# Performance work log

Measured on AMD Instinct MI355X. Metric: run time of the kernel, lower is better.

## Reference

```python
import jax, jax.numpy as jnp
import numpy as np

B, D, L, T, K = 16, 256, 256, 1000, 3
DW, DC = 4, 2  # dim_w, dim_c
CH = 8         # ConvSwishBlock out channels (10 = 1 start + 1 end + 8)


def swish(x):
    return x * jax.nn.sigmoid(x)


def setup_inputs() -> dict:
    key = jax.random.key(0)
    ks = jax.random.split(key, 12)
    # durations ~ U[1,6] per phone -> sum ~ 3.5*L ~ 896 <= T
    durations = 1.0 + 5.0 * jax.random.uniform(ks[0], (B, L), dtype=jnp.float32)
    phoneme = jax.random.normal(ks[1], (B, D, L), dtype=jnp.float32)
    # True = padded phone position
    phone_len = L - (jnp.arange(B) % 4) * 16
    phoneme_mask = (jnp.arange(L)[None, :] >= phone_len[:, None])[:, None, :]
    durations = jnp.where(phoneme_mask[:, 0, :], 0.0, durations)
    s = 0.02
    p = {
        'proj_w_W': s * jax.random.normal(ks[2], (D, D)), 'proj_w_b': jnp.zeros((D,)),
        'conv_w_W': s * jax.random.normal(ks[3], (CH, D, K)), 'conv_w_b': jnp.zeros((CH,)),
        'mlp_w_W': s * jax.random.normal(ks[4], (2 + CH, DW)), 'mlp_w_b': jnp.zeros((DW,)),
        'lin_w_W': s * jax.random.normal(ks[5], (D * DW, D)), 'lin_w_b': jnp.zeros((D,)),
        'proj_c_W': s * jax.random.normal(ks[6], (D, D)), 'proj_c_b': jnp.zeros((D,)),
        'conv_c_W': s * jax.random.normal(ks[7], (CH, D, K)), 'conv_c_b': jnp.zeros((CH,)),
        'mlp_c_W': s * jax.random.normal(ks[8], (2 + CH, DC)), 'mlp_c_b': jnp.zeros((DC,)),
        'lin_c_W': s * jax.random.normal(ks[9], (DW * DC, D)), 'lin_c_b': jnp.zeros((D,)),
    }
    return {'durations': durations, 'phoneme': phoneme, 'phoneme_mask': phoneme_mask, **p}


def _conv_branch(x, phone_pad, projW, projb, convW, convb):
    # x: (B, D, L). 1x1 conv projection, then K-wide 'same' conv to CH channels, swish, mask.
    x = jnp.einsum('od,bdl->bol', projW, x) + projb[None, :, None]
    h = jax.lax.conv_general_dilated(x, convW, (1,), 'SAME',
                                     dimension_numbers=('NCH', 'OIH', 'NCH'))
    h = swish(h + convb[None, :, None])
    h = jnp.where(phone_pad[:, None, :], 0.0, h)
    return h.transpose(0, 2, 1)  # (B, L, CH)


def _forward(durations, phoneme, phoneme_mask,
             proj_w_W, proj_w_b, conv_w_W, conv_w_b, mlp_w_W, mlp_w_b, lin_w_W, lin_w_b,
             proj_c_W, proj_c_b, conv_c_W, conv_c_b, mlp_c_W, mlp_c_b, lin_c_W, lin_c_b):
    phone_pad = phoneme_mask[:, 0, :]                       # (B, L) True = pad
    frame_len = jnp.clip(jnp.round(jnp.sum(durations, -1)), 0, T).astype(jnp.int32)
    frame_pad = jnp.arange(T)[None, :] >= frame_len[:, None]  # (B, T) True = pad
    attn_pad = frame_pad[:, :, None] | phone_pad[:, None, :]  # (B, T, L)

    sd = jnp.cumsum(durations, -1)                          # (B, L) cumulative end times
    sk = sd - durations                                     # (B, L) start times
    t = jnp.arange(1, T + 1, dtype=durations.dtype)
    S = jnp.where(attn_pad, 0.0, t[None, :, None] - sk[:, None, :])                    # (B,T,L)
    E = jnp.where(attn_pad, 0.0, jnp.broadcast_to(sd[:, None, :], attn_pad.shape)
                  - sk[:, None, :])                                                    # (B,T,L)

    # W branch: per-(frame, phone) attention weights over phones
    h_w = _conv_branch(phoneme, phone_pad, proj_w_W, proj_w_b, conv_w_W, conv_w_b)     # (B,L,CH)
    feat_w = jnp.concatenate(
        [S[..., None], E[..., None], jnp.broadcast_to(h_w[:, None], (B, T, L, CH))], -1)
    w = swish(feat_w @ mlp_w_W + mlp_w_b)                   # (B, T, L, DW)
    w = jnp.where(phone_pad[:, None, :, None], -jnp.inf, w)
    w = jax.nn.softmax(w, axis=2)                           # softmax over phones
    w = jnp.where(frame_pad[:, :, None, None], 0.0, w)

    # C branch: auxiliary per-(frame, phone) context
    h_c = _conv_branch(phoneme, phone_pad, proj_c_W, proj_c_b, conv_c_W, conv_c_b)
    feat_c = jnp.concatenate(
        [S[..., None], E[..., None], jnp.broadcast_to(h_c[:, None], (B, T, L, CH))], -1)
    c = swish(feat_c @ mlp_c_W + mlp_c_b)                   # (B, T, L, DC)

    # combine: wh = einsum over phones with phoneme features, wc with c matrix
    wh = jnp.einsum('btnq,bnh->btqh', w, phoneme.transpose(0, 2, 1))  # (B,T,DW,D)
    wh = wh.reshape(B, T, DW * D) @ lin_w_W + lin_w_b                 # (B,T,D)
    wc = jnp.einsum('btnq,btnp->btqp', w, c)                          # (B,T,DW,DC)
    wc = wc.reshape(B, T, DW * DC) @ lin_c_W + lin_c_b                # (B,T,D)
    return wh + wc


def reference(durations, phoneme, phoneme_mask,
              proj_w_W, proj_w_b, conv_w_W, conv_w_b, mlp_w_W, mlp_w_b, lin_w_W, lin_w_b,
              proj_c_W, proj_c_b, conv_c_W, conv_c_b, mlp_c_W, mlp_c_b, lin_c_W, lin_c_b):
    return _forward(durations, phoneme, phoneme_mask,
                    proj_w_W, proj_w_b, conv_w_W, conv_w_b, mlp_w_W, mlp_w_b, lin_w_W, lin_w_b,
                    proj_c_W, proj_c_b, conv_c_W, conv_c_b, mlp_c_W, mlp_c_b, lin_c_W, lin_c_b)
```

## Files before the change

### kernel.cpp

```cpp
#include <hip/hip_runtime.h>


typedef short v8s __attribute__((ext_vector_type(8)));
typedef _Float16 v8h __attribute__((ext_vector_type(8)));
typedef float f4 __attribute__((ext_vector_type(4)));

__device__ __forceinline__ float bf2f(unsigned short h) {
  return __uint_as_float(((unsigned int)h) << 16);
}
__device__ __forceinline__ unsigned short f2bf(float f) {
  unsigned int u = __float_as_uint(f);
  u = (u + 0x7FFFu + ((u >> 16) & 1u)) >> 16;
  return (unsigned short)u;
}
__device__ __forceinline__ float swishf(float x) {
  return x * __builtin_amdgcn_rcpf(1.f + __expf(-x));
}

__global__ __launch_bounds__(256) void k_prep(
    const float* __restrict__ dur, const float* __restrict__ ph,
    const float* __restrict__ liWw,
    const float* __restrict__ cvWw, const float* __restrict__ pjWw,
    const float* __restrict__ pjbw,
    const float* __restrict__ cvWc, const float* __restrict__ pjWc,
    const float* __restrict__ pjbc,
    float* __restrict__ sk, int* __restrict__ frame_len,
    unsigned short* __restrict__ Mb, float* __restrict__ bK,
    unsigned short* __restrict__ LWT, unsigned short* __restrict__ phT) {
  __shared__ float sm[32 * 33];
  int blk = blockIdx.x, tid = threadIdx.x;
  if (blk < 16) {
    int b = blk, l = tid;
    float d = dur[b * 256 + l];
    sm[l] = d;
    __syncthreads();
    for (int off = 1; off < 256; off <<= 1) {
      float v = (l >= off) ? sm[l - off] : 0.f;
      __syncthreads();
      sm[l] += v;
      __syncthreads();
    }
    sk[b * 256 + l] = sm[l] - d;
    if (l == 255) {
      int fl = (int)rintf(sm[255]);
      frame_len[b] = min(max(fl, 0), 1000);
    }
  } else if (blk < 64) {
    int x = blk - 16;
    int br = x / 24, ck = x % 24;
    int ch = ck / 3, k = ck % 3;
    const float* convW = br ? cvWc : cvWw;
    const float* projW = br ? pjWc : pjWw;
    const float* projb = br ? pjbc : pjbw;
    int d = tid;
    float acc = 0.f;
    for (int o = 0; o < 256; o++)
      acc += convW[ch * 768 + o * 3 + k] * projW[o * 256 + d];
    Mb[(br * 24 + ck) * 256 + d] = f2bf(acc);
    if (d == 0) {
      float bb = 0.f;
      for (int o = 0; o < 256; o++)
        bb += convW[ch * 768 + o * 3 + k] * projb[o];
      bK[br * 24 + ck] = bb;
    }
  } else if (blk < 320) {
    int idx = blk - 64;
    int kt = idx & 31, ot = idx >> 5;
    int tx = tid & 31, ty = tid >> 5;
#pragma unroll
    for (int r = 0; r < 4; r++) {
      int row = ty + r * 8;
      sm[row * 33 + tx] = liWw[(size_t)(kt * 32 + row) * 256 + ot * 32 + tx];
    }
    __syncthreads();
#pragma unroll
    for (int r = 0; r < 4; r++) {
      int row = ty + r * 8;
      LWT[(size_t)(ot * 32 + row) * 1024 + kt * 32 + tx] =
          f2bf(sm[tx * 33 + row]);
    }
  } else {
    int idx = blk - 320;
    int ht = idx & 7, lt = (idx >> 3) & 7, b = idx >> 6;
    int tx = tid & 31, ty = tid >> 5;
#pragma unroll
    for (int r = 0; r < 4; r++) {
      int row = ty + r * 8;
      sm[row * 33 + tx] =
          ph[(size_t)b * 65536 + (size_t)(ht * 32 + row) * 256 + lt * 32 + tx];
    }
    __syncthreads();
#pragma unroll
    for (int r = 0; r < 4; r++) {
      int row = ty + r * 8;
      phT[(size_t)b * 65536 + (size_t)(lt * 32 + row) * 256 + ht * 32 + tx] =
          f2bf(sm[tx * 33 + row]);
    }
  }
}

__global__ __launch_bounds__(256) void k_convG(
    const unsigned short* __restrict__ phT, const unsigned short* __restrict__ Mb,
    const float* __restrict__ bK, const float* __restrict__ cvbw,
    const float* __restrict__ cvbc, const float* __restrict__ dur,
    const unsigned short* __restrict__ LWT,
    float* __restrict__ hw, float* __restrict__ hc,
    _Float16* __restrict__ G) {
  __shared__ __align__(16) float C[256 * 49];
  int blk = blockIdx.x;
  int tid = threadIdx.x, wave = tid >> 6, lane = tid & 63;
  int quad = lane >> 4, col = lane & 15;
  if (blk < 16) {
    int b = blk;
    int l0 = wave * 64;
    const unsigned short* Ab = phT + (size_t)b * 65536;
    f4 acc[4][3] = {};
#pragma unroll
    for (int k0 = 0; k0 < 256; k0 += 32) {
      v8s af[4], bf[3];
#pragma unroll
      for (int lt = 0; lt < 4; lt++)
        af[lt] = *(const v8s*)(Ab + (size_t)(l0 + lt * 16 + col) * 256 + k0 + quad * 8);
#pragma unroll
      for (int ct = 0; ct < 3; ct++)
        bf[ct] = *(const v8s*)(Mb + (size_t)(ct * 16 + col) * 256 + k0 + quad * 8);
#pragma unroll
      for (int lt = 0; lt < 4; lt++)
#pragma unroll
        for (int ct = 0; ct < 3; ct++)
          acc[lt][ct] = __builtin_amdgcn_mfma_f32_16x16x32_bf16(af[lt], bf[ct],
                                                                acc[lt][ct], 0, 0, 0);
    }
#pragma unroll
    for (int lt = 0; lt < 4; lt++)
#pragma unroll
      for (int ct = 0; ct < 3; ct++)
#pragma unroll
        for (int r = 0; r < 4; r++)
          C[(l0 + lt * 16 + quad * 4 + r) * 49 + ct * 16 + col] = acc[lt][ct][r];
    __syncthreads();
    int l = tid;
    float dv = dur[b * 256 + l];
    bool vld = (dv != 0.f);
#pragma unroll
    for (int br = 0; br < 2; br++) {
      const float* convb = br ? cvbc : cvbw;
      float* dst = br ? hc : hw;
#pragma unroll
      for (int ch = 0; ch < 8; ch++) {
        int ck = br * 24 + ch * 3;
        float v = convb[ch] + bK[ck + 1] + C[l * 49 + ck + 1];
        if (l > 0) v += bK[ck + 0] + C[(l - 1) * 49 + ck + 0];
        if (l < 255) v += bK[ck + 2] + C[(l + 1) * 49 + ck + 2];
        v = swishf(v);
        dst[((size_t)(b * 256 + l)) * 8 + ch] = vld ? v : 0.f;
      }
    }
  } else {
    int idx = blk - 16;
    int b = idx >> 4;
    int sub = idx & 15;
    int q = sub >> 2, quadr = sub & 3;
    int mo = (quadr >> 1) * 128, nl = (quadr & 1) * 128;
    int wm = (wave & 1) * 64, wn = (wave >> 1) * 64;
    const unsigned short* Ag = LWT + (size_t)q * 256;
    const unsigned short* Bg = phT + (size_t)b * 65536;
    f4 acc[4][4] = {};
#pragma unroll
    for (int k0 = 0; k0 < 256; k0 += 32) {
      v8s af[4], bf[4];
#pragma unroll
      for (int mt = 0; mt < 4; mt++)
        af[mt] = *(const v8s*)(Ag + (size_t)(mo + wm + mt * 16 + col) * 1024 +
                               k0 + quad * 8);
#pragma unroll
      for (int nt = 0; nt < 4; nt++)
        bf[nt] = *(const v8s*)(Bg + (size_t)(nl + wn + nt * 16 + col) * 256 +
                               k0 + quad * 8);
#pragma unroll
      for (int mt = 0; mt < 4; mt++)
#pragma unroll
        for (int nt = 0; nt < 4; nt++)
          acc[mt][nt] = __builtin_amdgcn_mfma_f32_16x16x32_bf16(af[mt], bf[nt],
                                                                acc[mt][nt], 0, 0, 0);
    }
    _Float16* Gb = G + (size_t)b * 262144 + q * 256;
#pragma unroll
    for (int mt = 0; mt < 4; mt++)
#pragma unroll
      for (int r = 0; r < 4; r++) {
        int orow = mo + wm + mt * 16 + quad * 4 + r;
#pragma unroll
        for (int nt = 0; nt < 4; nt++) {
          int lcol = nl + wn + nt * 16 + col;
          Gb[(size_t)orow * 1024 + lcol] = (_Float16)acc[mt][nt][r];
        }
      }
  }
}

__global__ __launch_bounds__(256) void k_soft(
    const float* __restrict__ dur, const float* __restrict__ sk,
    const int* __restrict__ frame_len,
    const float* __restrict__ hw, const float* __restrict__ hc,
    const float* __restrict__ mlpWw, const float* __restrict__ mlpbw,
    const float* __restrict__ mlpWc, const float* __restrict__ mlpbc,
    _Float16* __restrict__ w, float* __restrict__ wc) {
  __shared__ __align__(16) float4 Lbw4[272];
  __shared__ __align__(16) float4 Laux4[272];
  __shared__ float4 wredM[4];
  int b = blockIdx.y;
  int t0 = blockIdx.x * 16;
  int tid = threadIdx.x, wave = tid >> 6, lane = tid & 63;

  {
    int l = tid;
    float4 a0 = *(const float4*)&hw[((size_t)(b * 256 + l)) * 8];
    float4 a1 = *(const float4*)&hw[((size_t)(b * 256 + l)) * 8 + 4];
    float4 c0 = *(const float4*)&hc[((size_t)(b * 256 + l)) * 8];
    float4 c1 = *(const float4*)&hc[((size_t)(b * 256 + l)) * 8 + 4];
    float hwv[8] = {a0.x, a0.y, a0.z, a0.w, a1.x, a1.y, a1.z, a1.w};
    float hcv[8] = {c0.x, c0.y, c0.z, c0.w, c1.x, c1.y, c1.z, c1.w};
    float dl = dur[b * 256 + l];
    float skl = sk[b * 256 + l];
    float msk = (dl != 0.f) ? 1.f : 0.f;
    float A[4];
#pragma unroll
    for (int q = 0; q < 4; q++) {
      float a = mlpbw[q] + dl * mlpWw[4 + q] - skl * mlpWw[q];
#pragma unroll
      for (int ch = 0; ch < 8; ch++) a += hwv[ch] * mlpWw[(2 + ch) * 4 + q];
      A[q] = (msk != 0.f) ? a : -1e30f;
    }
    float bb0 = mlpbc[0] + dl * mlpWc[2] - skl * mlpWc[0];
    float bb1 = mlpbc[1] + dl * mlpWc[3] - skl * mlpWc[1];
#pragma unroll
    for (int ch = 0; ch < 8; ch++) {
      bb0 += hcv[ch] * mlpWc[(2 + ch) * 2 + 0];
      bb1 += hcv[ch] * mlpWc[(2 + ch) * 2 + 1];
    }
    int li = l + (l >> 4);
    float4 Av = {A[0], A[1], A[2], A[3]};
    Lbw4[li] = Av;
    float4 xv = {bb0, bb1, msk, 0.f};
    Laux4[li] = xv;
    float m0 = A[0], m1 = A[1], m2 = A[2], m3 = A[3];
#pragma unroll
    for (int off = 1; off < 64; off <<= 1) {
      m0 = fmaxf(m0, __shfl_xor(m0, off));
      m1 = fmaxf(m1, __shfl_xor(m1, off));
      m2 = fmaxf(m2, __shfl_xor(m2, off));
      m3 = fmaxf(m3, __shfl_xor(m3, off));
    }
    if (lane == 0) {
      float4 mv = {m0, m1, m2, m3};
      wredM[wave] = mv;
    }
  }
  __syncthreads();
  float4 W0 = wredM[0], W1 = wredM[1], W2 = wredM[2], W3 = wredM[3];
  float maxA[4] = {fmaxf(fmaxf(W0.x, W1.x), fmaxf(W2.x, W3.x)),
                   fmaxf(fmaxf(W0.y, W1.y), fmaxf(W2.y, W3.y)),
                   fmaxf(fmaxf(W0.z, W1.z), fmaxf(W2.z, W3.z)),
                   fmaxf(fmaxf(W0.w, W1.w), fmaxf(W2.w, W3.w))};

  int fl = frame_len[b];
  int tl = wave * 4 + (lane >> 4);
  int l16 = lane & 15;
  int t = t0 + tl;
  bool live = (t < fl);
  float tp1 = (float)(t + 1);
  float mw0[4] = {mlpWw[0], mlpWw[1], mlpWw[2], mlpWw[3]};
  float mc0 = mlpWc[0], mc1 = mlpWc[1];
  float m[4];
#pragma unroll
  for (int q = 0; q < 4; q++)
    m[q] = live ? fmaxf(maxA[q] + tp1 * mw0[q], 0.f) : 1e30f;

  float s[4] = {}, pw[4][2] = {{}, {}, {}, {}};
  v8h eh[4][2];
  int lbase = l16 * 17;
#pragma unroll
  for (int j = 0; j < 16; j++) {
    float4 A4 = Lbw4[lbase + j];
    float4 ax = Laux4[lbase + j];
    float cp0 = swishf(ax.x + tp1 * mc0);
    float cp1 = swishf(ax.y + tp1 * mc1);
    float Aq[4] = {A4.x, A4.y, A4.z, A4.w};
#pragma unroll
    for (int q = 0; q < 4; q++) {
      float z = Aq[q] + tp1 * mw0[q];
      float e = __expf(swishf(z) - m[q]) * ax.z;
      eh[q][j >> 3][j & 7] = (_Float16)e;
      s[q] += e;
      pw[q][0] += e * cp0;
      pw[q][1] += e * cp1;
    }
  }
#pragma unroll
  for (int off = 1; off < 16; off <<= 1) {
#pragma unroll
    for (int q = 0; q < 4; q++) {
      s[q] += __shfl_xor(s[q], off);
      pw[q][0] += __shfl_xor(pw[q][0], off);
      pw[q][1] += __shfl_xor(pw[q][1], off);
    }
  }
  size_t base = ((size_t)b * 1024 + t) * 1024;
#pragma unroll
  for (int q = 0; q < 4; q++) {
    float iv = live ? __builtin_amdgcn_rcpf(s[q]) : 0.f;
    _Float16 ivh = (_Float16)iv;
    v8h w0 = eh[q][0] * ivh;
    v8h w1 = eh[q][1] * ivh;
    *(v8h*)(w + base + q * 256 + l16 * 16) = w0;
    *(v8h*)(w + base + q * 256 + l16 * 16 + 8) = w1;
    if (l16 == 0 && t < 1000) {
      wc[((size_t)(b * 1000 + t)) * 8 + q * 2 + 0] = pw[q][0] * iv;
      wc[((size_t)(b * 1000 + t)) * 8 + q * 2 + 1] = pw[q][1] * iv;
    }
  }
}

__global__ __launch_bounds__(256) void k_out(const _Float16* __restrict__ w,
                                             const _Float16* __restrict__ G,
                                             const float* __restrict__ lwb,
                                             const float* __restrict__ lcb,
                                             const float* __restrict__ LC,
                                             const float* __restrict__ wc,
                                             float* __restrict__ out) {
  int b = blockIdx.y;
  int t0 = (blockIdx.x >> 1) * 32;
  int o0 = (blockIdx.x & 1) * 128;
  int tid = threadIdx.x, wave = tid >> 6, lane = tid & 63;
  int quad = lane >> 4, col = lane & 15;
  __shared__ __align__(16) _Float16 Asm[32 * 40];
  __shared__ __align__(16) _Float16 Bsm[128 * 40];
  __shared__ float bias_s[128];
  __shared__ float lcs[8][128];
  __shared__ float wcs[32][8];

  for (int i = tid; i < 128; i += 256) bias_s[i] = lwb[o0 + i] + lcb[o0 + i];
  for (int i = tid; i < 1024; i += 256)
    lcs[i >> 7][i & 127] = LC[(i >> 7) * 256 + o0 + (i & 127)];
  {
    int r = tid >> 3, j = tid & 7;
    int t = t0 + r;
    wcs[r][j] = (t < 1000) ? wc[((size_t)(b * 1000 + t)) * 8 + j] : 0.f;
  }

  bool aload = tid < 128;
  int arow = tid >> 2, aseg = tid & 3;
  const _Float16* Ag =
      w + (size_t)b * 1048576 + (size_t)(t0 + arow) * 1024 + aseg * 8;
  _Float16* Al = Asm + arow * 40 + aseg * 8;
  int brow = wave * 32 + (lane >> 2), bseg = lane & 3;
  const _Float16* Bg0 =
      G + (size_t)b * 262144 + (size_t)(o0 + brow) * 1024 + bseg * 8;
  const _Float16* Bg1 = Bg0 + 16 * 1024;
  _Float16* Bl0 = Bsm + brow * 40 + bseg * 8;
  _Float16* Bl1 = Bl0 + 16 * 40;

  int wm = (wave & 1) * 16, wn = (wave >> 1) * 64;
  f4 acc[4] = {};
  uint4 ra = {0, 0, 0, 0};
  if (aload) ra = *(const uint4*)Ag;
  uint4 rb0 = *(const uint4*)Bg0;
  uint4 rb1 = *(const uint4*)Bg1;
  for (int k0 = 0; k0 < 1024; k0 += 32) {
    __syncthreads();
    if (aload) *(uint4*)Al = ra;
    *(uint4*)Bl0 = rb0;
    *(uint4*)Bl1 = rb1;
    __syncthreads();
    if (k0 + 32 < 1024) {
      if (aload) ra = *(const uint4*)(Ag + k0 + 32);
      rb0 = *(const uint4*)(Bg0 + k0 + 32);
      rb1 = *(const uint4*)(Bg1 + k0 + 32);
    }
    v8h af = *(const v8h*)(Asm + (wm + col) * 40 + quad * 8);
    v8h bf[4];
#pragma unroll
    for (int nt = 0; nt < 4; nt++)
      bf[nt] = *(const v8h*)(Bsm + (wn + nt * 16 + col) * 40 + quad * 8);
#pragma unroll
    for (int nt = 0; nt < 4; nt++)
      acc[nt] = __builtin_amdgcn_mfma_f32_16x16x32_f16(af, bf[nt],
                                                       acc[nt], 0, 0, 0);
  }
#pragma unroll
  for (int r = 0; r < 4; r++) {
    int lrow = wm + quad * 4 + r;
    int trow = t0 + lrow;
    if (trow < 1000) {
      float4 wa = *(const float4*)&wcs[lrow][0];
      float4 wb = *(const float4*)&wcs[lrow][4];
      float wcl[8] = {wa.x, wa.y, wa.z, wa.w, wb.x, wb.y, wb.z, wb.w};
#pragma unroll
      for (int nt = 0; nt < 4; nt++) {
        int oc = wn + nt * 16 + col;
        float v = acc[nt][r] + bias_s[oc];
#pragma unroll
        for (int jj = 0; jj < 8; jj++) v = fmaf(wcl[jj], lcs[jj][oc], v);
        out[((size_t)(b * 1000 + trow)) * 256 + o0 + oc] = v;
      }
    }
  }
}

extern "C" void kernel_launch(void* const* d_in, const int* in_sizes, int n_in,
                              void* d_out, int out_size, void* d_ws, size_t ws_size,
                              hipStream_t stream) {
  const float* dur  = (const float*)d_in[0];
  const float* ph   = (const float*)d_in[1];
  const float* pjWw = (const float*)d_in[3];
  const float* pjbw = (const float*)d_in[4];
  const float* cvWw = (const float*)d_in[5];
  const float* cvbw = (const float*)d_in[6];
  const float* mlWw = (const float*)d_in[7];
  const float* mlbw = (const float*)d_in[8];
  const float* liWw = (const float*)d_in[9];
  const float* libw = (const float*)d_in[10];
  const float* pjWc = (const float*)d_in[11];
  const float* pjbc = (const float*)d_in[12];
  const float* cvWc = (const float*)d_in[13];
  const float* cvbc = (const float*)d_in[14];
  const float* mlWc = (const float*)d_in[15];
  const float* mlbc = (const float*)d_in[16];
  const float* liWc = (const float*)d_in[17];
  const float* libc = (const float*)d_in[18];
  float* out = (float*)d_out;

  float* f = (float*)d_ws;
  size_t o = 0;
  float* sk = f + o;            o += 4096;
  int* fl = (int*)(f + o);      o += 16;
  float* bK = f + o;            o += 64;
  unsigned short* Mb = (unsigned short*)(f + o); o += 6144;
  float* hw = f + o;            o += 16 * 256 * 8;
  float* hc = f + o;            o += 16 * 256 * 8;
  float* wc = f + o;            o += 16 * 1000 * 8;
  _Float16* G = (_Float16*)(f + o);              o += 2097152;
  _Float16* w = (_Float16*)(f + o);              o += 8388608;
  unsigned short* phT = (unsigned short*)(f + o); o += 524288;
  unsigned short* LWT = (unsigned short*)(f + o); o += 131072;

  k_prep<<<1344, 256, 0, stream>>>(dur, ph, liWw, cvWw, pjWw, pjbw, cvWc, pjWc,
                                   pjbc, sk, fl, Mb, bK, LWT, phT);
  k_convG<<<272, 256, 0, stream>>>(phT, Mb, bK, cvbw, cvbc, dur, LWT, hw, hc, G);
  k_soft<<<dim3(63, 16), 256, 0, stream>>>(dur, sk, fl, hw, hc, mlWw, mlbw,
                                           mlWc, mlbc, w, wc);
  k_out<<<dim3(64, 16), 256, 0, stream>>>(w, G, libw, libc, liWc, wc, out);
}
```

Baseline: 175.0 us.

## Enlarge prep transpose tiles, parallelize bias reduction, remap block-to-batch order

The prep kernel's transposes now use 64x64 tiles instead of 32x32, cutting its grid from 1344 to 384 blocks. The conv-weight fold stages conv weights in shared memory, and the serial single-thread bias sum becomes a wave-shuffle reduction. k_convG and k_out now remap block indices so consecutive blocks alternate batches across the likely XCD round-robin dispatch, and k_out moves to a flat 1D grid. These changes aim to shorten the prep kernel and improve cache locality. The cost is larger shared memory per prep block, which may lower occupancy.

```diff
diff --git a/kernel.cpp b/kernel.cpp
--- a/kernel.cpp
+++ b/kernel.cpp
@@ -27,7 +27,7 @@
     float* __restrict__ sk, int* __restrict__ frame_len,
     unsigned short* __restrict__ Mb, float* __restrict__ bK,
     unsigned short* __restrict__ LWT, unsigned short* __restrict__ phT) {
-  __shared__ float sm[32 * 33];
+  __shared__ float sm[64 * 65];
   int blk = blockIdx.x, tid = threadIdx.x;
   if (blk < 16) {
     int b = blk, l = tid;
@@ -52,49 +52,55 @@
     const float* convW = br ? cvWc : cvWw;
     const float* projW = br ? pjWc : pjWw;
     const float* projb = br ? pjbc : pjbw;
+    float* cwS = sm;
+    float* red = sm + 256;
+    cwS[tid] = convW[ch * 768 + tid * 3 + k];
+    __syncthreads();
     int d = tid;
     float acc = 0.f;
+#pragma unroll 4
     for (int o = 0; o < 256; o++)
-      acc += convW[ch * 768 + o * 3 + k] * projW[o * 256 + d];
+      acc = fmaf(cwS[o], projW[o * 256 + d], acc);
     Mb[(br * 24 + ck) * 256 + d] = f2bf(acc);
-    if (d == 0) {
-      float bb = 0.f;
-      for (int o = 0; o < 256; o++)
-        bb += convW[ch * 768 + o * 3 + k] * projb[o];
-      bK[br * 24 + ck] = bb;
-    }
-  } else if (blk < 320) {
+    float p = cwS[tid] * projb[tid];
+#pragma unroll
+    for (int off = 1; off < 64; off <<= 1) p += __shfl_xor(p, off);
+    if ((tid & 63) == 0) red[tid >> 6] = p;
+    __syncthreads();
+    if (tid == 0) bK[br * 24 + ck] = red[0] + red[1] + red[2] + red[3];
+  } else if (blk < 128) {
     int idx = blk - 64;
-    int kt = idx & 31, ot = idx >> 5;
-    int tx = tid & 31, ty = tid >> 5;
-#pragma unroll
-    for (int r = 0; r < 4; r++) {
-      int row = ty + r * 8;
-      sm[row * 33 + tx] = liWw[(size_t)(kt * 32 + row) * 256 + ot * 32 + tx];
-    }
-    __syncthreads();
-#pragma unroll
-    for (int r = 0; r < 4; r++) {
-      int row = ty + r * 8;
-      LWT[(size_t)(ot * 32 + row) * 1024 + kt * 32 + tx] =
-          f2bf(sm[tx * 33 + row]);
+    int kt = idx & 15, ot = idx >> 4;
+    int col = tid & 63, rq = tid >> 6;
+#pragma unroll
+    for (int it = 0; it < 16; it++) {
+      int row = it * 4 + rq;
+      sm[row * 65 + col] = liWw[(size_t)(kt * 64 + row) * 256 + ot * 64 + col];
+    }
+    __syncthreads();
+#pragma unroll
+    for (int it = 0; it < 16; it++) {
+      int row = it * 4 + rq;
+      LWT[(size_t)(ot * 64 + row) * 1024 + kt * 64 + col] =
+          f2bf(sm[col * 65 + row]);
     }
   } else {
-    int idx = blk - 320;
-    int ht = idx & 7, lt = (idx >> 3) & 7, b = idx >> 6;
-    int tx = tid & 31, ty = tid >> 5;
-#pragma unroll
-    for (int r = 0; r < 4; r++) {
-      int row = ty + r * 8;
-      sm[row * 33 + tx] =
-          ph[(size_t)b * 65536 + (size_t)(ht * 32 + row) * 256 + lt * 32 + tx];
-    }
-    __syncthreads();
-#pragma unroll
-    for (int r = 0; r < 4; r++) {
-      int row = ty + r * 8;
-      phT[(size_t)b * 65536 + (size_t)(lt * 32 + row) * 256 + ht * 32 + tx] =
-          f2bf(sm[tx * 33 + row]);
+    int idx = blk - 128;
+    int b = idx >> 4, ht = (idx >> 2) & 3, lt = idx & 3;
+    int col = tid & 63, rq = tid >> 6;
+    const float* src = ph + (size_t)b * 65536;
+    unsigned short* dst = phT + (size_t)b * 65536;
+#pragma unroll
+    for (int it = 0; it < 16; it++) {
+      int row = it * 4 + rq;
+      sm[row * 65 + col] = src[(size_t)(ht * 64 + row) * 256 + lt * 64 + col];
+    }
+    __syncthreads();
+#pragma unroll
+    for (int it = 0; it < 16; it++) {
+      int row = it * 4 + rq;
+      dst[(size_t)(lt * 64 + row) * 256 + ht * 64 + col] =
+          f2bf(sm[col * 65 + row]);
     }
   }
 }
@@ -158,8 +164,8 @@
     }
   } else {
     int idx = blk - 16;
-    int b = idx >> 4;
-    int sub = idx & 15;
+    int b = ((idx & 7) << 1) | ((idx >> 3) & 1);
+    int sub = idx >> 4;
     int q = sub >> 2, quadr = sub & 3;
     int mo = (quadr >> 1) * 128, nl = (quadr & 1) * 128;
     int wm = (wave & 1) * 64, wn = (wave >> 1) * 64;
@@ -329,9 +335,11 @@
                                              const float* __restrict__ LC,
                                              const float* __restrict__ wc,
                                              float* __restrict__ out) {
-  int b = blockIdx.y;
-  int t0 = (blockIdx.x >> 1) * 32;
-  int o0 = (blockIdx.x & 1) * 128;
+  int n = blockIdx.x;
+  int b = ((n & 7) << 1) | ((n >> 3) & 1);
+  int rem = n >> 4;
+  int t0 = (rem >> 1) * 32;
+  int o0 = (rem & 1) * 128;
   int tid = threadIdx.x, wave = tid >> 6, lane = tid & 63;
   int quad = lane >> 4, col = lane & 15;
   __shared__ __align__(16) _Float16 Asm[32 * 40];
@@ -445,10 +453,10 @@
   unsigned short* phT = (unsigned short*)(f + o); o += 524288;
   unsigned short* LWT = (unsigned short*)(f + o); o += 131072;
 
-  k_prep<<<1344, 256, 0, stream>>>(dur, ph, liWw, cvWw, pjWw, pjbw, cvWc, pjWc,
-                                   pjbc, sk, fl, Mb, bK, LWT, phT);
+  k_prep<<<384, 256, 0, stream>>>(dur, ph, liWw, cvWw, pjWw, pjbw, cvWc, pjWc,
+                                  pjbc, sk, fl, Mb, bK, LWT, phT);
   k_convG<<<272, 256, 0, stream>>>(phT, Mb, bK, cvbw, cvbc, dur, LWT, hw, hc, G);
   k_soft<<<dim3(63, 16), 256, 0, stream>>>(dur, sk, fl, hw, hc, mlWw, mlbw,
                                            mlWc, mlbc, w, wc);
-  k_out<<<dim3(64, 16), 256, 0, stream>>>(w, G, libw, libc, liWc, wc, out);
-}
+  k_out<<<1024, 256, 0, stream>>>(w, G, libw, libc, liWc, wc, out);
+}
```

Result: slower. 181.4 us (+3.7%).
